# Kernel optimization log

Hardware: AMD Instinct MI355X
Metric: run time of the kernel (lower is better)

Reference implementation:

```python
import jax, jax.numpy as jnp
import numpy as np
from jax.ops import segment_sum

NUM_NODES = 100000
NUM_GRAPHS = 256


def gcn_conv(x, src, dst, W, b, num_nodes):
    """PyG GCNConv: add self-loops, symmetric deg^-1/2 normalization,
    out = scatter_add(norm * (xW)[src]) + b."""
    h = x @ W  # [N, H]
    loop = jnp.arange(num_nodes, dtype=src.dtype)
    s = jnp.concatenate([src, loop])
    d = jnp.concatenate([dst, loop])
    deg = segment_sum(jnp.ones_like(d, dtype=h.dtype), d, num_segments=num_nodes)
    dinv = jnp.where(deg > 0, jax.lax.rsqrt(deg), 0.0)
    norm = dinv[s] * dinv[d]  # [E+N]
    msg = h[s] * norm[:, None]
    return segment_sum(msg, d, num_segments=num_nodes) + b


def global_mean_pool(x, batch, num_graphs):
    summed = segment_sum(x, batch, num_segments=num_graphs)
    cnt = segment_sum(jnp.ones_like(batch, dtype=x.dtype), batch, num_segments=num_graphs)
    return summed / jnp.maximum(cnt, 1.0)[:, None]


def setup_inputs() -> dict:
    key = jax.random.key(0)
    ks = jax.random.split(key, 8)
    N, E, F_in, H = NUM_NODES, 3200000, 128, 64
    x = jax.random.normal(ks[0], (N, F_in), dtype=jnp.float32)
    edge_index = jax.random.randint(ks[1], (2, E), 0, N, dtype=jnp.int64)
    batch = jnp.sort(jax.random.randint(ks[2], (N,), 0, NUM_GRAPHS, dtype=jnp.int64))
    def glorot(k, shape):
        fan = shape[0] + shape[1]
        return jax.random.uniform(k, shape, jnp.float32, -1.0, 1.0) * np.sqrt(6.0 / fan)
    return {
        "x": x, "edge_index": edge_index, "batch": batch,
        "W1": glorot(ks[3], (F_in, H)), "b1": jnp.zeros((H,), jnp.float32),
        "W2": glorot(ks[4], (H, H)),   "b2": jnp.zeros((H,), jnp.float32),
        "W3": glorot(ks[5], (H, H)),   "b3": jnp.zeros((H,), jnp.float32),
        "Wl": glorot(ks[6], (H, 2)),   "bl": jnp.zeros((2,), jnp.float32),
    }


def reference(x, edge_index, batch, W1, b1, W2, b2, W3, b3, Wl, bl):
    src, dst = edge_index[0], edge_index[1]
    # Dropout acts as identity in eval mode; reference is deterministic.
    h = jax.nn.relu(gcn_conv(x, src, dst, W1, b1, NUM_NODES))
    h = jax.nn.relu(gcn_conv(h, src, dst, W2, b2, NUM_NODES))
    h = jax.nn.relu(gcn_conv(h, src, dst, W3, b3, NUM_NODES))
    g = global_mean_pool(h, batch, NUM_GRAPHS)  # [G, H]
    return g @ Wl + bl  # [G, 2]
```

## Files before the change

### kernel.cpp

```cpp
#include <hip/hip_runtime.h>
#include <hip/hip_bf16.h>
#include <cstdint>
#include <cstddef>

static constexpr int N_NODES = 100000;
static constexpr int N_GRAPHS = 256;
static constexpr int HF = 64;

#define SCAN_T 256
#define SCAN_E 8
#define SCAN_CHUNK (SCAN_T * SCAN_E)

#define BSHIFT 9
#define BNODES 512
#define ECHUNK 4096
#define SRCBITS 17

typedef unsigned short u16;
typedef unsigned int u32;

__global__ void scan1_k(const int* __restrict__ in, int* __restrict__ out,
                        int* __restrict__ sums, int n) {
    __shared__ int lds[SCAN_T];
    int t = threadIdx.x;
    int base = blockIdx.x * SCAN_CHUNK + t * SCAN_E;
    int v[SCAN_E];
    int s = 0;
#pragma unroll
    for (int i = 0; i < SCAN_E; ++i) {
        int idx = base + i;
        int x = (idx < n) ? in[idx] : 0;
        v[i] = s; s += x;
    }
    lds[t] = s; __syncthreads();
    for (int off = 1; off < SCAN_T; off <<= 1) {
        int a = (t >= off) ? lds[t - off] : 0;
        __syncthreads();
        lds[t] += a;
        __syncthreads();
    }
    int excl = (t == 0) ? 0 : lds[t - 1];
    if (t == SCAN_T - 1) sums[blockIdx.x] = lds[SCAN_T - 1];
#pragma unroll
    for (int i = 0; i < SCAN_E; ++i) {
        int idx = base + i;
        if (idx < n) out[idx] = excl + v[i];
    }
}

__global__ void scan2_k(int* __restrict__ sums, int nb) {
    __shared__ int lds[SCAN_T];
    int t = threadIdx.x;
    lds[t] = (t < nb) ? sums[t] : 0;
    __syncthreads();
    for (int off = 1; off < SCAN_T; off <<= 1) {
        int a = (t >= off) ? lds[t - off] : 0;
        __syncthreads();
        lds[t] += a;
        __syncthreads();
    }
    int excl = (t == 0) ? 0 : lds[t - 1];
    if (t < nb) sums[t] = excl;
}

__global__ void scan3_k(int* __restrict__ out, const int* __restrict__ sums, int n) {
    int idx = blockIdx.x * blockDim.x + threadIdx.x;
    if (idx < n) out[idx] += sums[idx / SCAN_CHUNK];
}

__global__ void bhist_k(const int* __restrict__ dst, int* __restrict__ cnt,
                        int E, int nblk, int NB) {
    __shared__ int c[256];
    int t = threadIdx.x;
    c[t] = 0;
    __syncthreads();
    int base = blockIdx.x * ECHUNK;
    int m = min(ECHUNK, E - base);
    for (int i = t; i < m; i += 256) atomicAdd(&c[dst[base + i] >> BSHIFT], 1);
    __syncthreads();
    if (t < NB) cnt[t * nblk + blockIdx.x] = c[t];
}

__global__ void scatter_k(const int* __restrict__ src, const int* __restrict__ dst,
                          const int* __restrict__ scn, int* __restrict__ es,
                          int E, int nblk, int NB) {
    __shared__ int offs[256];
    int t = threadIdx.x;
    if (t < NB) offs[t] = scn[t * nblk + blockIdx.x];
    __syncthreads();
    int base = blockIdx.x * ECHUNK;
    int m = min(ECHUNK, E - base);
    for (int i = t; i < m; i += 256) {
        int e = base + i;
        int d = dst[e];
        int b = d >> BSHIFT;
        int p = atomicAdd(&offs[b], 1);
        es[p] = ((d & (BNODES - 1)) << SRCBITS) | src[e];
    }
}

__global__ __launch_bounds__(512) void fill2_k(const int* __restrict__ es,
                                               const int* __restrict__ scn,
                                               int* __restrict__ rowp, int* __restrict__ deg,
                                               float* __restrict__ dinv, int* __restrict__ col,
                                               int E, int nblk, int NB, int N) {
    __shared__ int ldeg[BNODES];
    __shared__ int rp[BNODES];
    __shared__ int tmp[BNODES];
    int b = blockIdx.x, t = threadIdx.x;
    int ebase = scn[b * nblk];
    int eend = (b + 1 < NB) ? scn[(b + 1) * nblk] : E;
    int d0 = b << BSHIFT;
    int nd = min(BNODES, N - d0);
    ldeg[t] = 0;
    __syncthreads();
    for (int e = ebase + t; e < eend; e += 512) atomicAdd(&ldeg[((u32)es[e]) >> SRCBITS], 1);
    __syncthreads();
    int a = ldeg[t];
    tmp[t] = a;
    __syncthreads();
    for (int off = 1; off < BNODES; off <<= 1) {
        int v = (t >= off) ? tmp[t - off] : 0;
        __syncthreads();
        tmp[t] += v;
        __syncthreads();
    }
    rp[t] = tmp[t] - a;
    __syncthreads();
    if (t < nd) {
        int d = d0 + t;
        rowp[d] = ebase + rp[t];
        deg[d] = a;
        dinv[d] = rsqrtf((float)(a + 1));
    }
    ldeg[t] = 0;
    __syncthreads();
    for (int e = ebase + t; e < eend; e += 512) {
        u32 w = (u32)es[e];
        int li = w >> SRCBITS;
        int p = atomicAdd(&ldeg[li], 1);
        col[ebase + rp[li] + p] = (int)(w & ((1u << SRCBITS) - 1));
    }
}

__global__ void wtrans_k(const float* __restrict__ W, float4* __restrict__ W4, int total) {
    int idx = blockIdx.x * blockDim.x + threadIdx.x;
    if (idx >= total) return;
    int k4 = idx >> 6, c = idx & 63;
    W4[idx] = make_float4(W[(4 * k4 + 0) * HF + c], W[(4 * k4 + 1) * HF + c],
                          W[(4 * k4 + 2) * HF + c], W[(4 * k4 + 3) * HF + c]);
}

template <int K>
__global__ __launch_bounds__(256, 4) void gemm4_k(const float* __restrict__ in,
                                                  const float4* __restrict__ W4,
                                                  const float* __restrict__ dinv,
                                                  __hip_bfloat16* __restrict__ u, int n) {
    __shared__ float4 Wl[16 * HF];
    __shared__ float4 Xl[64 * 17];
    int t = threadIdx.x;
    int wave = t >> 6, lane = t & 63;
    int rb = blockIdx.x * 64;
    float acc[16];
#pragma unroll
    for (int i = 0; i < 16; ++i) acc[i] = 0.f;
    constexpr int NC = K / 64;
#pragma unroll 1
    for (int kc = 0; kc < NC; ++kc) {
        const float4* Wc = W4 + kc * 16 * HF;
#pragma unroll 1
        for (int i = t; i < 16 * HF; i += 256) Wl[i] = Wc[i];
        {
            int r = t >> 4, q = t & 15;
#pragma unroll 1
            for (int i = 0; i < 4; ++i) {
                int row = r + i * 16;
                int gr = rb + row;
                float4 v = (gr < n)
                    ? *(const float4*)(in + (size_t)gr * K + kc * 64 + q * 4)
                    : make_float4(0.f, 0.f, 0.f, 0.f);
                Xl[row * 17 + q] = v;
            }
        }
        __syncthreads();
        int r0 = wave * 16;
#pragma unroll 1
        for (int k4 = 0; k4 < 16; ++k4) {
            float4 w = Wl[k4 * HF + lane];
#pragma unroll
            for (int r = 0; r < 16; ++r) {
                float4 v = Xl[(r0 + r) * 17 + k4];
                acc[r] = fmaf(v.x, w.x, fmaf(v.y, w.y, fmaf(v.z, w.z, fmaf(v.w, w.w, acc[r]))));
            }
        }
        __syncthreads();
    }
#pragma unroll 1
    for (int r = 0; r < 16; ++r) {
        int row = rb + wave * 16 + r;
        if (row < n) u[(size_t)row * HF + lane] = __float2bfloat16(acc[r] * dinv[row]);
    }
}

__global__ __launch_bounds__(256) void agg2_k(const u32* __restrict__ u,
                                              const int* __restrict__ col,
                                              const int* __restrict__ rowp,
                                              const int* __restrict__ deg,
                                              const float* __restrict__ dinv,
                                              const float* __restrict__ bias,
                                              float* __restrict__ out, int n) {
    int t = threadIdx.x;
    int wave = t >> 6, lane = t & 63;
    int sl = lane & 31;
    int v = blockIdx.x * 8 + wave * 2 + (lane >> 5);
    if (v >= n) return;
    u32 q = u[(size_t)v * 32 + sl];
    float ax = __uint_as_float(q << 16);
    float ay = __uint_as_float(q & 0xffff0000u);
    int start = rowp[v];
    int nE = deg[v];
    for (int e = 0; e < nE;) {
        int m = min(32, nE - e);
        int c = (sl < m) ? col[start + e + sl] : 0;
        int i = 0;
        for (; i + 8 <= m; i += 8) {
            int s0 = __shfl(c, i, 32),     s1 = __shfl(c, i + 1, 32);
            int s2 = __shfl(c, i + 2, 32), s3 = __shfl(c, i + 3, 32);
            int s4 = __shfl(c, i + 4, 32), s5 = __shfl(c, i + 5, 32);
            int s6 = __shfl(c, i + 6, 32), s7 = __shfl(c, i + 7, 32);
            u32 q0 = u[(size_t)s0 * 32 + sl];
            u32 q1 = u[(size_t)s1 * 32 + sl];
            u32 q2 = u[(size_t)s2 * 32 + sl];
            u32 q3 = u[(size_t)s3 * 32 + sl];
            u32 q4 = u[(size_t)s4 * 32 + sl];
            u32 q5 = u[(size_t)s5 * 32 + sl];
            u32 q6 = u[(size_t)s6 * 32 + sl];
            u32 q7 = u[(size_t)s7 * 32 + sl];
            ax += __uint_as_float(q0 << 16);  ay += __uint_as_float(q0 & 0xffff0000u);
            ax += __uint_as_float(q1 << 16);  ay += __uint_as_float(q1 & 0xffff0000u);
            ax += __uint_as_float(q2 << 16);  ay += __uint_as_float(q2 & 0xffff0000u);
            ax += __uint_as_float(q3 << 16);  ay += __uint_as_float(q3 & 0xffff0000u);
            ax += __uint_as_float(q4 << 16);  ay += __uint_as_float(q4 & 0xffff0000u);
            ax += __uint_as_float(q5 << 16);  ay += __uint_as_float(q5 & 0xffff0000u);
            ax += __uint_as_float(q6 << 16);  ay += __uint_as_float(q6 & 0xffff0000u);
            ax += __uint_as_float(q7 << 16);  ay += __uint_as_float(q7 & 0xffff0000u);
        }
        for (; i < m; ++i) {
            int s = __shfl(c, i, 32);
            u32 qq = u[(size_t)s * 32 + sl];
            ax += __uint_as_float(qq << 16);
            ay += __uint_as_float(qq & 0xffff0000u);
        }
        e += m;
    }
    float dv = dinv[v];
    float2 o;
    o.x = fmaxf(fmaf(ax, dv, bias[2 * sl]), 0.f);
    o.y = fmaxf(fmaf(ay, dv, bias[2 * sl + 1]), 0.f);
    ((float2*)out)[(size_t)v * 32 + sl] = o;
}

__device__ __forceinline__ int lower_bound_i(const int* a, int n, int key) {
    int lo = 0, hi = n;
    while (lo < hi) { int mid = (lo + hi) >> 1; if (a[mid] < key) lo = mid + 1; else hi = mid; }
    return lo;
}

__global__ void pool_head_k(const float* __restrict__ h, const int* __restrict__ batch,
                            const float* __restrict__ Wl, const float* __restrict__ bl,
                            float* __restrict__ out, int n) {
    __shared__ float ssum[4][HF];
    __shared__ float smean[HF];
    int g = blockIdx.x;
    int wave = threadIdx.x >> 6, lane = threadIdx.x & 63;
    int start = lower_bound_i(batch, n, g);
    int end = lower_bound_i(batch, n, g + 1);
    float acc = 0.f;
    for (int v = start + wave; v < end; v += 4) acc += h[(size_t)v * HF + lane];
    ssum[wave][lane] = acc;
    __syncthreads();
    if (wave == 0) {
        float s = ssum[0][lane] + ssum[1][lane] + ssum[2][lane] + ssum[3][lane];
        float cnt = (float)(end - start);
        smean[lane] = s / fmaxf(cnt, 1.f);
    }
    __syncthreads();
    if (threadIdx.x < 2) {
        float o = bl[threadIdx.x];
        for (int j = 0; j < HF; ++j) o += smean[j] * Wl[j * 2 + threadIdx.x];
        out[g * 2 + threadIdx.x] = o;
    }
}

extern "C" void kernel_launch(void* const* d_in, const int* in_sizes, int n_in,
                              void* d_out, int out_size, void* d_ws, size_t ws_size,
                              hipStream_t stream) {
    const float* x     = (const float*)d_in[0];
    const int*   ei    = (const int*)d_in[1];
    const int*   batch = (const int*)d_in[2];
    const float* W1 = (const float*)d_in[3];
    const float* b1 = (const float*)d_in[4];
    const float* W2 = (const float*)d_in[5];
    const float* b2 = (const float*)d_in[6];
    const float* W3 = (const float*)d_in[7];
    const float* b3 = (const float*)d_in[8];
    const float* Wl = (const float*)d_in[9];
    const float* bl = (const float*)d_in[10];
    float* outp = (float*)d_out;

    const int N = N_NODES;
    const int E = in_sizes[1] / 2;
    const int NB = (N + BNODES - 1) >> BSHIFT;
    const int NBLK = (E + ECHUNK - 1) / ECHUNK;
    const int M = NB * NBLK;

    char* ws = (char*)d_ws;
    size_t off = 0;
    auto alloc = [&](size_t bytes) {
        void* p = ws + off;
        off = (off + bytes + 255) & ~size_t(255);
        return p;
    };
    size_t ubytes = (size_t)N * HF * 2;
    if ((size_t)E * 4 > ubytes) ubytes = (size_t)E * 4;
    float*  P    = (float*)alloc((size_t)N * HF * 4);
    void*   Uv   = alloc(ubytes);
    int*    colA = (int*)alloc((size_t)E * 4);
    int*    deg  = (int*)alloc((size_t)N * 4);
    float*  dinv = (float*)alloc((size_t)N * 4);
    int*    rowp = (int*)alloc((size_t)N * 4);
    int*    cnt  = (int*)alloc((size_t)M * 4);
    int*    scn  = (int*)alloc((size_t)M * 4);
    int*    sums = (int*)alloc(4096);
    float4* W4_1 = (float4*)alloc((size_t)(128 / 4) * HF * 16);
    float4* W4_2 = (float4*)alloc((size_t)(64 / 4) * HF * 16);
    float4* W4_3 = (float4*)alloc((size_t)(64 / 4) * HF * 16);
    __hip_bfloat16* U = (__hip_bfloat16*)Uv;
    u32* U32 = (u32*)Uv;
    int* es  = (int*)Uv;
    (void)ws_size; (void)n_in; (void)out_size;

    const int* src = ei;
    const int* dst = ei + E;

    bhist_k<<<NBLK, 256, 0, stream>>>(dst, cnt, E, NBLK, NB);
    int nb = (M + SCAN_CHUNK - 1) / SCAN_CHUNK;
    scan1_k<<<nb, SCAN_T, 0, stream>>>(cnt, scn, sums, M);
    scan2_k<<<1, SCAN_T, 0, stream>>>(sums, nb);
    scan3_k<<<(M + 255) / 256, 256, 0, stream>>>(scn, sums, M);
    scatter_k<<<NBLK, 256, 0, stream>>>(src, dst, scn, es, E, NBLK, NB);
    fill2_k<<<NB, 512, 0, stream>>>(es, scn, rowp, deg, dinv, colA, E, NBLK, NB, N);

    wtrans_k<<<(32 * HF + 255) / 256, 256, 0, stream>>>(W1, W4_1, 32 * HF);
    wtrans_k<<<(16 * HF + 255) / 256, 256, 0, stream>>>(W2, W4_2, 16 * HF);
    wtrans_k<<<(16 * HF + 255) / 256, 256, 0, stream>>>(W3, W4_3, 16 * HF);

    int gRow8  = (N + 7) / 8;
    int gRow64 = (N + 63) / 64;
    gemm4_k<128><<<gRow64, 256, 0, stream>>>(x, W4_1, dinv, U, N);
    agg2_k<<<gRow8, 256, 0, stream>>>(U32, colA, rowp, deg, dinv, b1, P, N);
    gemm4_k<64><<<gRow64, 256, 0, stream>>>(P, W4_2, dinv, U, N);
    agg2_k<<<gRow8, 256, 0, stream>>>(U32, colA, rowp, deg, dinv, b2, P, N);
    gemm4_k<64><<<gRow64, 256, 0, stream>>>(P, W4_3, dinv, U, N);
    agg2_k<<<gRow8, 256, 0, stream>>>(U32, colA, rowp, deg, dinv, b3, P, N);

    pool_head_k<<<N_GRAPHS, 256, 0, stream>>>(P, batch, Wl, bl, outp, N);
}
```

Before: 385.2 us.

## Keep GEMM weights in registers and widen aggregation gathers to 8-byte loads

The dense transform kernel no longer stages W and X tiles in LDS. Each lane holds its weight column chunk in registers and reads input rows straight from global memory, with wave-uniform broadcast loads and no block barriers. The aggregation kernel now gives each node 16 lanes, each loading 64 bits (four bf16 values), so one wave handles four nodes and issues wider gather requests per edge. This trades LDS reuse and coalesced tile loads for higher register pressure and scalar-broadcast global reads.

```diff
diff --git a/kernel.cpp b/kernel.cpp
--- a/kernel.cpp
+++ b/kernel.cpp
@@ -18,6 +18,7 @@
 
 typedef unsigned short u16;
 typedef unsigned int u32;
+typedef unsigned long long u64;
 
 __global__ void scan1_k(const int* __restrict__ in, int* __restrict__ out,
                         int* __restrict__ sums, int n) {
@@ -152,57 +153,44 @@
 }
 
 template <int K>
-__global__ __launch_bounds__(256, 4) void gemm4_k(const float* __restrict__ in,
-                                                  const float4* __restrict__ W4,
-                                                  const float* __restrict__ dinv,
-                                                  __hip_bfloat16* __restrict__ u, int n) {
-    __shared__ float4 Wl[16 * HF];
-    __shared__ float4 Xl[64 * 17];
+__global__ __launch_bounds__(256) void gemm5_k(const float* __restrict__ in,
+                                               const float4* __restrict__ W4,
+                                               const float* __restrict__ dinv,
+                                               __hip_bfloat16* __restrict__ u, int n) {
     int t = threadIdx.x;
     int wave = t >> 6, lane = t & 63;
-    int rb = blockIdx.x * 64;
+    int rb = blockIdx.x * 64 + wave * 16;
     float acc[16];
 #pragma unroll
     for (int i = 0; i < 16; ++i) acc[i] = 0.f;
     constexpr int NC = K / 64;
 #pragma unroll 1
     for (int kc = 0; kc < NC; ++kc) {
+        float4 w[16];
         const float4* Wc = W4 + kc * 16 * HF;
+#pragma unroll
+        for (int k4 = 0; k4 < 16; ++k4) w[k4] = Wc[k4 * HF + lane];
 #pragma unroll 1
-        for (int i = t; i < 16 * HF; i += 256) Wl[i] = Wc[i];
-        {
-            int r = t >> 4, q = t & 15;
-#pragma unroll 1
-            for (int i = 0; i < 4; ++i) {
-                int row = r + i * 16;
-                int gr = rb + row;
-                float4 v = (gr < n)
-                    ? *(const float4*)(in + (size_t)gr * K + kc * 64 + q * 4)
-                    : make_float4(0.f, 0.f, 0.f, 0.f);
-                Xl[row * 17 + q] = v;
+        for (int r = 0; r < 16; ++r) {
+            int row = rb + r;
+            if (row >= n) break;
+            const float4* xr = (const float4*)(in + (size_t)row * K + kc * 64);
+#pragma unroll 8
+            for (int k4 = 0; k4 < 16; ++k4) {
+                float4 v = xr[k4];
+                acc[r] = fmaf(v.x, w[k4].x, fmaf(v.y, w[k4].y,
+                         fmaf(v.z, w[k4].z, fmaf(v.w, w[k4].w, acc[r]))));
             }
         }
-        __syncthreads();
-        int r0 = wave * 16;
-#pragma unroll 1
-        for (int k4 = 0; k4 < 16; ++k4) {
-            float4 w = Wl[k4 * HF + lane];
-#pragma unroll
-            for (int r = 0; r < 16; ++r) {
-                float4 v = Xl[(r0 + r) * 17 + k4];
-                acc[r] = fmaf(v.x, w.x, fmaf(v.y, w.y, fmaf(v.z, w.z, fmaf(v.w, w.w, acc[r]))));
-            }
-        }
-        __syncthreads();
     }
 #pragma unroll 1
     for (int r = 0; r < 16; ++r) {
-        int row = rb + wave * 16 + r;
+        int row = rb + r;
         if (row < n) u[(size_t)row * HF + lane] = __float2bfloat16(acc[r] * dinv[row]);
     }
 }
 
-__global__ __launch_bounds__(256) void agg2_k(const u32* __restrict__ u,
+__global__ __launch_bounds__(256) void agg3_k(const u64* __restrict__ u,
                                               const int* __restrict__ col,
                                               const int* __restrict__ rowp,
                                               const int* __restrict__ deg,
@@ -210,54 +198,64 @@
                                               const float* __restrict__ bias,
                                               float* __restrict__ out, int n) {
     int t = threadIdx.x;
-    int wave = t >> 6, lane = t & 63;
-    int sl = lane & 31;
-    int v = blockIdx.x * 8 + wave * 2 + (lane >> 5);
+    int ql = t & 15;
+    int v = blockIdx.x * 16 + (t >> 4);
     if (v >= n) return;
-    u32 q = u[(size_t)v * 32 + sl];
-    float ax = __uint_as_float(q << 16);
-    float ay = __uint_as_float(q & 0xffff0000u);
+    u64 q = u[(size_t)v * 16 + ql];
+    u32 lo = (u32)q, hi = (u32)(q >> 32);
+    float a0 = __uint_as_float(lo << 16);
+    float a1 = __uint_as_float(lo & 0xffff0000u);
+    float a2 = __uint_as_float(hi << 16);
+    float a3 = __uint_as_float(hi & 0xffff0000u);
     int start = rowp[v];
     int nE = deg[v];
     for (int e = 0; e < nE;) {
-        int m = min(32, nE - e);
-        int c = (sl < m) ? col[start + e + sl] : 0;
+        int m = min(16, nE - e);
+        int c = (ql < m) ? col[start + e + ql] : 0;
         int i = 0;
         for (; i + 8 <= m; i += 8) {
-            int s0 = __shfl(c, i, 32),     s1 = __shfl(c, i + 1, 32);
-            int s2 = __shfl(c, i + 2, 32), s3 = __shfl(c, i + 3, 32);
-            int s4 = __shfl(c, i + 4, 32), s5 = __shfl(c, i + 5, 32);
-            int s6 = __shfl(c, i + 6, 32), s7 = __shfl(c, i + 7, 32);
-            u32 q0 = u[(size_t)s0 * 32 + sl];
-            u32 q1 = u[(size_t)s1 * 32 + sl];
-            u32 q2 = u[(size_t)s2 * 32 + sl];
-            u32 q3 = u[(size_t)s3 * 32 + sl];
-            u32 q4 = u[(size_t)s4 * 32 + sl];
-            u32 q5 = u[(size_t)s5 * 32 + sl];
-            u32 q6 = u[(size_t)s6 * 32 + sl];
-            u32 q7 = u[(size_t)s7 * 32 + sl];
-            ax += __uint_as_float(q0 << 16);  ay += __uint_as_float(q0 & 0xffff0000u);
-            ax += __uint_as_float(q1 << 16);  ay += __uint_as_float(q1 & 0xffff0000u);
-            ax += __uint_as_float(q2 << 16);  ay += __uint_as_float(q2 & 0xffff0000u);
-            ax += __uint_as_float(q3 << 16);  ay += __uint_as_float(q3 & 0xffff0000u);
-            ax += __uint_as_float(q4 << 16);  ay += __uint_as_float(q4 & 0xffff0000u);
-            ax += __uint_as_float(q5 << 16);  ay += __uint_as_float(q5 & 0xffff0000u);
-            ax += __uint_as_float(q6 << 16);  ay += __uint_as_float(q6 & 0xffff0000u);
-            ax += __uint_as_float(q7 << 16);  ay += __uint_as_float(q7 & 0xffff0000u);
+            int s0 = __shfl(c, i, 16),     s1 = __shfl(c, i + 1, 16);
+            int s2 = __shfl(c, i + 2, 16), s3 = __shfl(c, i + 3, 16);
+            int s4 = __shfl(c, i + 4, 16), s5 = __shfl(c, i + 5, 16);
+            int s6 = __shfl(c, i + 6, 16), s7 = __shfl(c, i + 7, 16);
+            u64 q0 = u[(size_t)s0 * 16 + ql];
+            u64 q1 = u[(size_t)s1 * 16 + ql];
+            u64 q2 = u[(size_t)s2 * 16 + ql];
+            u64 q3 = u[(size_t)s3 * 16 + ql];
+            u64 q4 = u[(size_t)s4 * 16 + ql];
+            u64 q5 = u[(size_t)s5 * 16 + ql];
+            u64 q6 = u[(size_t)s6 * 16 + ql];
+            u64 q7 = u[(size_t)s7 * 16 + ql];
+#pragma unroll
+            for (int j = 0; j < 8; ++j) {
+                u64 qq = j == 0 ? q0 : j == 1 ? q1 : j == 2 ? q2 : j == 3 ? q3
+                       : j == 4 ? q4 : j == 5 ? q5 : j == 6 ? q6 : q7;
+                u32 l = (u32)qq, h = (u32)(qq >> 32);
+                a0 += __uint_as_float(l << 16);
+                a1 += __uint_as_float(l & 0xffff0000u);
+                a2 += __uint_as_float(h << 16);
+                a3 += __uint_as_float(h & 0xffff0000u);
+            }
         }
         for (; i < m; ++i) {
-            int s = __shfl(c, i, 32);
-            u32 qq = u[(size_t)s * 32 + sl];
-            ax += __uint_as_float(qq << 16);
-            ay += __uint_as_float(qq & 0xffff0000u);
+            int s = __shfl(c, i, 16);
+            u64 qq = u[(size_t)s * 16 + ql];
+            u32 l = (u32)qq, h = (u32)(qq >> 32);
+            a0 += __uint_as_float(l << 16);
+            a1 += __uint_as_float(l & 0xffff0000u);
+            a2 += __uint_as_float(h << 16);
+            a3 += __uint_as_float(h & 0xffff0000u);
         }
         e += m;
     }
     float dv = dinv[v];
-    float2 o;
-    o.x = fmaxf(fmaf(ax, dv, bias[2 * sl]), 0.f);
-    o.y = fmaxf(fmaf(ay, dv, bias[2 * sl + 1]), 0.f);
-    ((float2*)out)[(size_t)v * 32 + sl] = o;
+    float4 bb = ((const float4*)bias)[ql];
+    float4 o;
+    o.x = fmaxf(fmaf(a0, dv, bb.x), 0.f);
+    o.y = fmaxf(fmaf(a1, dv, bb.y), 0.f);
+    o.z = fmaxf(fmaf(a2, dv, bb.z), 0.f);
+    o.w = fmaxf(fmaf(a3, dv, bb.w), 0.f);
+    ((float4*)out)[(size_t)v * 16 + ql] = o;
 }
 
 __device__ __forceinline__ int lower_bound_i(const int* a, int n, int key) {
@@ -336,7 +334,7 @@
     float4* W4_2 = (float4*)alloc((size_t)(64 / 4) * HF * 16);
     float4* W4_3 = (float4*)alloc((size_t)(64 / 4) * HF * 16);
     __hip_bfloat16* U = (__hip_bfloat16*)Uv;
-    u32* U32 = (u32*)Uv;
+    u64* U64 = (u64*)Uv;
     int* es  = (int*)Uv;
     (void)ws_size; (void)n_in; (void)out_size;
 
@@ -355,14 +353,14 @@
     wtrans_k<<<(16 * HF + 255) / 256, 256, 0, stream>>>(W2, W4_2, 16 * HF);
     wtrans_k<<<(16 * HF + 255) / 256, 256, 0, stream>>>(W3, W4_3, 16 * HF);
 
-    int gRow8  = (N + 7) / 8;
+    int gRow16 = (N + 15) / 16;
     int gRow64 = (N + 63) / 64;
-    gemm4_k<128><<<gRow64, 256, 0, stream>>>(x, W4_1, dinv, U, N);
-    agg2_k<<<gRow8, 256, 0, stream>>>(U32, colA, rowp, deg, dinv, b1, P, N);
-    gemm4_k<64><<<gRow64, 256, 0, stream>>>(P, W4_2, dinv, U, N);
-    agg2_k<<<gRow8, 256, 0, stream>>>(U32, colA, rowp, deg, dinv, b2, P, N);
-    gemm4_k<64><<<gRow64, 256, 0, stream>>>(P, W4_3, dinv, U, N);
-    agg2_k<<<gRow8, 256, 0, stream>>>(U32, colA, rowp, deg, dinv, b3, P, N);
+    gemm5_k<128><<<gRow64, 256, 0, stream>>>(x, W4_1, dinv, U, N);
+    agg3_k<<<gRow16, 256, 0, stream>>>(U64, colA, rowp, deg, dinv, b1, P, N);
+    gemm5_k<64><<<gRow64, 256, 0, stream>>>(P, W4_2, dinv, U, N);
+    agg3_k<<<gRow16, 256, 0, stream>>>(U64, colA, rowp, deg, dinv, b2, P, N);
+    gemm5_k<64><<<gRow64, 256, 0, stream>>>(P, W4_3, dinv, U, N);
+    agg3_k<<<gRow16, 256, 0, stream>>>(U64, colA, rowp, deg, dinv, b3, P, N);
 
     pool_head_k<<<N_GRAPHS, 256, 0, stream>>>(P, batch, Wl, bl, outp, N);
 }
```

After: 1.418 ms. +268.2%, slower.
